# Performance work log

Hardware: AMD Instinct MI355X
Metric: run time of the kernel (lower is better)

Reference implementation:

```python
import jax, jax.numpy as jnp
import numpy as np

N_NODES = 50000
N_EDGES = 800000
FEAT = 128
HID = 128
NUM_GRAPHS = 64
ODE_STEPS = 8   # fixed-step RK4 stand-in for adaptive odeint over CFG.ode_time_points
DEPTH = 1.0
EPS = 1e-5


def layer_norm(x, g, b):
    m = jnp.mean(x, axis=-1, keepdims=True)
    v = jnp.var(x, axis=-1, keepdims=True)
    return (x - m) * jax.lax.rsqrt(v + EPS) * g + b


def setup_inputs() -> dict:
    key = jax.random.key(0)
    ks = jax.random.split(key, 16)
    s = 1.0 / np.sqrt(FEAT)
    sh = 1.0 / np.sqrt(HID)
    inp = {
        "x": jax.random.normal(ks[0], (N_NODES, FEAT), jnp.float32),
        "edge_index": jax.random.randint(ks[1], (2, N_EDGES), 0, N_NODES, jnp.int64),
        "batch": jnp.sort(jax.random.randint(ks[2], (N_NODES,), 0, NUM_GRAPHS, jnp.int64)),
        "alpha": jnp.float32(0.8),
        "beta": jnp.float32(0.6),
        "phase": jnp.float32(0.7),
        "W_in": jax.random.normal(ks[3], (FEAT, HID), jnp.float32) * s,
        "b_in": jnp.zeros((HID,), jnp.float32),
        "g_in": jnp.ones((HID,), jnp.float32),
        "be_in": jnp.zeros((HID,), jnp.float32),
        "W_alt": jax.random.normal(ks[4], (FEAT, HID), jnp.float32) * s,
        "b_alt": jnp.zeros((HID,), jnp.float32),
        "g_alt": jnp.ones((HID,), jnp.float32),
        "be_alt": jnp.zeros((HID,), jnp.float32),
        "W_self": jax.random.normal(ks[5], (HID, HID), jnp.float32) * sh,
        "W_msg": jax.random.normal(ks[6], (HID, HID), jnp.float32) * sh,
        "b_ode": jnp.zeros((HID,), jnp.float32),
        "W_int": jax.random.normal(ks[7], (2 * HID, HID), jnp.float32) * sh / np.sqrt(2.0),
        "b_int": jnp.zeros((HID,), jnp.float32),
        "g_int": jnp.ones((HID,), jnp.float32),
        "be_int": jnp.zeros((HID,), jnp.float32),
        "W_out": jax.random.normal(ks[8], (HID, HID), jnp.float32) * sh,
        "b_out": jnp.zeros((HID,), jnp.float32),
    }
    return inp


def _forward(x, alpha, beta, phase,
             W_in, b_in, g_in, be_in,
             W_alt, b_alt, g_alt, be_alt,
             W_self, W_msg, b_ode,
             W_int, b_int, g_int, be_int,
             W_out, b_out,
             edge_index, batch):
    src, dst = edge_index[0], edge_index[1]
    # in-degree for mean aggregation (clamped to 1)
    deg = jax.ops.segment_sum(jnp.ones((src.shape[0],), jnp.float32), dst,
                              num_segments=N_NODES)
    deg = jnp.maximum(deg, 1.0)[:, None]

    # quantum amplitudes -> measurement probabilities (normalized)
    norm = jnp.sqrt(alpha ** 2 + beta ** 2)
    a, b = alpha / norm, beta / norm
    p0, p1 = a ** 2, b ** 2

    # two projection pathways in superposition
    h0 = jax.nn.gelu(layer_norm(x @ W_in + b_in, g_in, be_in))
    h1 = jax.nn.gelu(layer_norm(x @ W_alt + b_alt, g_alt, be_alt))
    h = jnp.sqrt(p0) * h0 + jnp.sqrt(p1) * h1  # [N, H]

    # Neural ODE: dh/dt = tanh(h W_self + mean_{j->i}(h_j W_msg) + b)
    def ode_f(h):
        msg = h[src] @ W_msg                       # [E, H] gather + GEMM
        agg = jax.ops.segment_sum(msg, dst, num_segments=N_NODES) / deg
        return jnp.tanh(h @ W_self + agg + b_ode)

    dt = jnp.float32(DEPTH / ODE_STEPS)

    def rk4_step(h, _):
        k1 = ode_f(h)
        k2 = ode_f(h + 0.5 * dt * k1)
        k3 = ode_f(h + 0.5 * dt * k2)
        k4 = ode_f(h + dt * k3)
        return h + (dt / 6.0) * (k1 + 2.0 * k2 + 2.0 * k3 + k4), None

    h, _ = jax.lax.scan(rk4_step, h, None, length=ODE_STEPS)

    # quantum interference mixing (conditional branch -> masked add)
    interf = 2.0 * jnp.sqrt(p0 * p1) * jnp.cos(phase)
    h_int = jnp.tanh(layer_norm(jnp.concatenate([h, h], axis=-1) @ W_int + b_int,
                                g_int, be_int))
    gate = jnp.where(jnp.abs(interf) > 0.01, interf, 0.0)
    h = h + gate * h_int

    # eval-mode collapse: if p1 >= p0, scale by Re(e^{i*phase}) = cos(phase)
    h = jnp.where(p0 > p1, h, h * jnp.cos(phase))

    h_out = h @ W_out + b_out

    # global mean pool over graphs
    cnt = jax.ops.segment_sum(jnp.ones((N_NODES,), jnp.float32), batch,
                              num_segments=NUM_GRAPHS)
    pooled = jax.ops.segment_sum(h_out, batch, num_segments=NUM_GRAPHS)
    return pooled / jnp.maximum(cnt, 1.0)[:, None]  # [NUM_GRAPHS, H]


def reference(x, edge_index, batch, alpha, beta, phase,
              W_in, b_in, g_in, be_in,
              W_alt, b_alt, g_alt, be_alt,
              W_self, W_msg, b_ode,
              W_int, b_int, g_int, be_int,
              W_out, b_out):
    return _forward(x, alpha, beta, phase,
                    W_in, b_in, g_in, be_in,
                    W_alt, b_alt, g_alt, be_alt,
                    W_self, W_msg, b_ode,
                    W_int, b_int, g_int, be_int,
                    W_out, b_out, edge_index, batch)
```

## Files before the change

### kernel.cpp

```cpp
#include <hip/hip_runtime.h>
#include <math.h>

#define NND 50000
#define NED 800000
#define HD  128
#define NG  64
#define MT  32

typedef __attribute__((ext_vector_type(8))) short short8v;
typedef __attribute__((ext_vector_type(4))) float float4v;
typedef __attribute__((ext_vector_type(2))) float float2v;

__device__ __forceinline__ float gelu_t(float x) {
  const float c = 0.7978845608028654f;
  float t = tanhf(c * (x + 0.044715f * x * x * x));
  return 0.5f * x * (1.0f + t);
}

__device__ __forceinline__ unsigned short f2bf(float f) {
  unsigned int u = __float_as_uint(f);
  u += 0x7FFFu + ((u >> 16) & 1u);
  return (unsigned short)(u >> 16);
}
__device__ __forceinline__ float bf2f(unsigned short s) {
  return __uint_as_float(((unsigned int)s) << 16);
}
__device__ __forceinline__ float bflo(unsigned int u) { return __uint_as_float(u << 16); }
__device__ __forceinline__ float bfhi(unsigned int u) { return __uint_as_float(u & 0xFFFF0000u); }

__global__ void k_hist(const int* __restrict__ dst, int* __restrict__ degi) {
  int e = blockIdx.x * 256 + threadIdx.x;
  if (e < NED) atomicAdd(&degi[dst[e]], 1);
}

__global__ __launch_bounds__(1024) void k_scan(
    const int* __restrict__ degi, int* __restrict__ rowptr,
    int* __restrict__ cursor, float* __restrict__ deginv) {
  __shared__ int wsum[16];
  int tid = threadIdx.x;
  int lane = tid & 63;
  int wid = tid >> 6;
  int running = 0;
  for (int base = 0; base < NND; base += 1024) {
    int idx = base + tid;
    int v = (idx < NND) ? degi[idx] : 0;
    int s = v;
#pragma unroll
    for (int o = 1; o < 64; o <<= 1) {
      int t = __shfl_up(s, o, 64);
      if (lane >= o) s += t;
    }
    if (lane == 63) wsum[wid] = s;
    __syncthreads();
    if (wid == 0) {
      int ws = (lane < 16) ? wsum[lane] : 0;
#pragma unroll
      for (int o = 1; o < 16; o <<= 1) {
        int t = __shfl_up(ws, o, 64);
        if (lane >= o) ws += t;
      }
      if (lane < 16) wsum[lane] = ws;
    }
    __syncthreads();
    int woff = wid ? wsum[wid - 1] : 0;
    int excl = running + woff + s - v;
    if (idx < NND) {
      rowptr[idx] = excl;
      cursor[idx] = excl;
      deginv[idx] = 1.0f / (float)max(v, 1);
    }
    int tot = wsum[15];
    __syncthreads();
    running += tot;
  }
  if (tid == 0) rowptr[NND] = running;
}

__global__ void k_scatter(const int* __restrict__ src, const int* __restrict__ dst,
                          int* __restrict__ cursor, unsigned short* __restrict__ cs16) {
  int e = blockIdx.x * 256 + threadIdx.x;
  if (e < NED) {
    int d = dst[e];
    int pos = atomicAdd(&cursor[d], 1);
    cs16[pos] = (unsigned short)src[e];
  }
}

__global__ void k_cnt(const int* __restrict__ batch, float* __restrict__ cnt) {
  int g = threadIdx.x;
  if (g >= NG) return;
  int lo, hi, ub_g, ub_gm1;
  lo = 0; hi = NND;
  while (lo < hi) { int mid = (lo + hi) >> 1; if (batch[mid] <= g) lo = mid + 1; else hi = mid; }
  ub_g = lo;
  if (g == 0) ub_gm1 = 0;
  else {
    lo = 0; hi = NND;
    int v = g - 1;
    while (lo < hi) { int mid = (lo + hi) >> 1; if (batch[mid] <= v) lo = mid + 1; else hi = mid; }
    ub_gm1 = lo;
  }
  cnt[g] = (float)(ub_g - ub_gm1);
}

__global__ void k_weffT(const float* __restrict__ Wint, unsigned short* __restrict__ weffT) {
  int i = blockIdx.x * 256 + threadIdx.x;
  if (i < 128 * 128) {
    int n = i >> 7, k = i & 127;
    weffT[i] = f2bf(Wint[k * 128 + n] + Wint[(k + 128) * 128 + n]);
  }
}

__global__ void k_prepOut(const float* __restrict__ Wout, unsigned short* __restrict__ WoutT) {
  int i = blockIdx.x * 256 + threadIdx.x;
  if (i < 128 * 128) {
    int n = i >> 7, k = i & 127;
    WoutT[i] = f2bf(Wout[k * 128 + n]);
  }
}

__global__ void k_prepB(const float* __restrict__ Wself, const float* __restrict__ Wmsg,
                        unsigned short* __restrict__ Bt) {
  int i = blockIdx.x * 256 + threadIdx.x;
  if (i < 128 * 256) {
    int n = i >> 8, k = i & 255;
    float w = (k < HD) ? Wself[k * HD + n] : Wmsg[(k - HD) * HD + n];
    Bt[i] = f2bf(w);
  }
}

__global__ void k_prepIn(const float* __restrict__ Win, const float* __restrict__ Walt,
                         unsigned short* __restrict__ BtIn) {
  int i = blockIdx.x * 256 + threadIdx.x;
  if (i < 2 * 128 * 128) {
    int p = i >> 14; int rem = i & 16383; int n = rem >> 7; int k = rem & 127;
    const float* W = p ? Walt : Win;
    BtIn[i] = f2bf(W[k * 128 + n]);
  }
}

__global__ __launch_bounds__(256) void k_init2(
    const float* __restrict__ x, const unsigned short* __restrict__ BtIn,
    const float* __restrict__ bin, const float* __restrict__ gin, const float* __restrict__ bein,
    const float* __restrict__ balt, const float* __restrict__ galt, const float* __restrict__ bealt,
    const float* __restrict__ alphap, const float* __restrict__ betap,
    unsigned short* __restrict__ hbf)
{
  __shared__ float red[4][16][2];
  __shared__ unsigned short gtile[2][16][64];
  int tid = threadIdx.x;
  int wave = tid >> 6;
  int lane = tid & 63;
  int l15 = lane & 15;
  int lhi = lane >> 4;
  int path = wave >> 1;
  int colBase = (wave & 1) * 64;
  int rowBase = blockIdx.x * 64;

  const unsigned short* Bp = BtIn + path * 128 * 128;
  short8v bfr[4][4];
#pragma unroll
  for (int t = 0; t < 4; ++t) {
    int n = colBase + t * 16 + l15;
#pragma unroll
    for (int s = 0; s < 4; ++s)
      bfr[t][s] = *(const short8v*)&Bp[n * 128 + s * 32 + lhi * 8];
  }

  const float* bvp = path ? balt : bin;
  const float* gp  = path ? galt : gin;
  const float* bep = path ? bealt : bein;
  float bv[4], gw[4], bew[4];
#pragma unroll
  for (int t = 0; t < 4; ++t) {
    int col = colBase + t * 16 + l15;
    bv[t] = bvp[col]; gw[t] = gp[col]; bew[t] = bep[col];
  }

  float al = alphap[0], btv = betap[0];
  float nrm = sqrtf(al * al + btv * btv);
  float w0 = fabsf(al) / nrm, w1 = fabsf(btv) / nrm;

  for (int rt = 0; rt < 4; ++rt) {
    int arow = rowBase + rt * 16 + l15; if (arow >= NND) arow = NND - 1;
    short8v afr[4];
#pragma unroll
    for (int s = 0; s < 4; ++s) {
      float4 xa = *(const float4*)&x[(size_t)arow * HD + s * 32 + lhi * 8];
      float4 xb = *(const float4*)&x[(size_t)arow * HD + s * 32 + lhi * 8 + 4];
      short8v f;
      f[0] = (short)f2bf(xa.x); f[1] = (short)f2bf(xa.y);
      f[2] = (short)f2bf(xa.z); f[3] = (short)f2bf(xa.w);
      f[4] = (short)f2bf(xb.x); f[5] = (short)f2bf(xb.y);
      f[6] = (short)f2bf(xb.z); f[7] = (short)f2bf(xb.w);
      afr[s] = f;
    }

    float4v acc[4];
#pragma unroll
    for (int t = 0; t < 4; ++t) acc[t] = (float4v){0.f, 0.f, 0.f, 0.f};
#pragma unroll
    for (int s = 0; s < 4; ++s) {
#pragma unroll
      for (int t = 0; t < 4; ++t)
        acc[t] = __builtin_amdgcn_mfma_f32_16x16x32_bf16(afr[s], bfr[t][s], acc[t], 0, 0, 0);
    }

    float z[4][4];
    float psum[4], psq[4];
#pragma unroll
    for (int r = 0; r < 4; ++r) {
      float s1 = 0.f, s2 = 0.f;
#pragma unroll
      for (int t = 0; t < 4; ++t) {
        float zz = acc[t][r] + bv[t];
        z[r][t] = zz;
        s1 += zz; s2 += zz * zz;
      }
#pragma unroll
      for (int m = 1; m < 16; m <<= 1) {
        s1 += __shfl_xor(s1, m, 16);
        s2 += __shfl_xor(s2, m, 16);
      }
      psum[r] = s1; psq[r] = s2;
    }
    if (l15 == 0) {
#pragma unroll
      for (int r = 0; r < 4; ++r) {
        red[wave][lhi * 4 + r][0] = psum[r];
        red[wave][lhi * 4 + r][1] = psq[r];
      }
    }
    __syncthreads();

    int pw = wave ^ 1;
    float gval[4][4];
#pragma unroll
    for (int r = 0; r < 4; ++r) {
      int rowl = lhi * 4 + r;
      float S = psum[r] + red[pw][rowl][0];
      float Q = psq[r]  + red[pw][rowl][1];
      float mean = S * (1.0f / 128.0f);
      float var  = Q * (1.0f / 128.0f) - mean * mean;
      float rs = rsqrtf(var + 1e-5f);
#pragma unroll
      for (int t = 0; t < 4; ++t)
        gval[r][t] = gelu_t((z[r][t] - mean) * rs * gw[t] + bew[t]);
    }

    if (path == 1) {
#pragma unroll
      for (int r = 0; r < 4; ++r)
#pragma unroll
        for (int t = 0; t < 4; ++t)
          gtile[wave & 1][lhi * 4 + r][t * 16 + l15] = f2bf(gval[r][t]);
    }
    __syncthreads();

    if (path == 0) {
#pragma unroll
      for (int r = 0; r < 4; ++r) {
        int m = rowBase + rt * 16 + lhi * 4 + r;
        if (m < NND) {
#pragma unroll
          for (int t = 0; t < 4; ++t) {
            float g1 = bf2f(gtile[wave & 1][lhi * 4 + r][t * 16 + l15]);
            float hv = w0 * gval[r][t] + w1 * g1;
            hbf[(size_t)m * HD + colBase + t * 16 + l15] = f2bf(hv);
          }
        }
      }
    }
    __syncthreads();
  }
}

__global__ __launch_bounds__(256) void k_gath2(
    const unsigned short* __restrict__ hbf,
    const unsigned char*  __restrict__ t8,
    unsigned short* __restrict__ usav,
    unsigned short* __restrict__ uT,
    const int* __restrict__ rowptr,
    const unsigned short* __restrict__ cs16,
    const float* __restrict__ deginv,
    int mode, float cu)
{
  int tid = threadIdx.x;
  int l16 = tid & 15;
  int grp = tid >> 4;
  int node = blockIdx.x * 16 + grp;
  if (node >= NND) return;
  int e0 = rowptr[node], e1 = rowptr[node + 1];
  float a0=0,a1=0,a2=0,a3=0,a4=0,a5=0,a6=0,a7=0;

  if (mode == 0) {
    for (int eb = e0; eb < e1; eb += 16) {
      int rem = e1 - eb;
      int ia = eb + l16; if (ia > e1 - 1) ia = e1 - 1;
      int my = cs16[ia];
      int n16 = (rem < 16) ? rem : 16;
#pragma unroll
      for (int j = 0; j < 16; ++j) {
        if (j < n16) {
          int s = __shfl(my, j, 16);
          uint4 v = *(const uint4*)&hbf[(size_t)s * HD + l16 * 8];
          a0 += bflo(v.x); a1 += bfhi(v.x); a2 += bflo(v.y); a3 += bfhi(v.y);
          a4 += bflo(v.z); a5 += bfhi(v.z); a6 += bflo(v.w); a7 += bfhi(v.w);
        }
      }
    }
  } else {
    for (int eb = e0; eb < e1; eb += 16) {
      int rem = e1 - eb;
      int ia = eb + l16; if (ia > e1 - 1) ia = e1 - 1;
      int my = cs16[ia];
      int n16 = (rem < 16) ? rem : 16;
      uint2 v[16];
#pragma unroll
      for (int j = 0; j < 16; ++j) {
        if (j < n16) {
          int s = __shfl(my, j, 16);
          v[j] = *(const uint2*)&t8[(size_t)s * HD + l16 * 8];
        }
      }
#pragma unroll
      for (int j = 0; j < 16; ++j) {
        if (j < n16) {
          float2v f0 = __builtin_amdgcn_cvt_pk_f32_fp8(v[j].x, false);
          float2v f1 = __builtin_amdgcn_cvt_pk_f32_fp8(v[j].x, true);
          float2v f2 = __builtin_amdgcn_cvt_pk_f32_fp8(v[j].y, false);
          float2v f3 = __builtin_amdgcn_cvt_pk_f32_fp8(v[j].y, true);
          a0 += f0[0]; a1 += f0[1]; a2 += f1[0]; a3 += f1[1];
          a4 += f2[0]; a5 += f2[1]; a6 += f3[0]; a7 += f3[1];
        }
      }
    }
  }

  float sc = deginv[node] * ((mode == 0) ? 1.0f : ((mode == 1) ? 0.125f : cu));
  size_t base = (size_t)node * HD + l16 * 8;
  float u0,u1,u2,u3,u4,u5,u6,u7;
  if (mode == 0) {
    u0=a0*sc; u1=a1*sc; u2=a2*sc; u3=a3*sc; u4=a4*sc; u5=a5*sc; u6=a6*sc; u7=a7*sc;
  } else {
    uint4 us = *(const uint4*)&usav[base];
    u0 = bflo(us.x) + a0*sc; u1 = bfhi(us.x) + a1*sc;
    u2 = bflo(us.y) + a2*sc; u3 = bfhi(us.y) + a3*sc;
    u4 = bflo(us.z) + a4*sc; u5 = bfhi(us.z) + a5*sc;
    u6 = bflo(us.w) + a6*sc; u7 = bfhi(us.w) + a7*sc;
  }
  uint4 o;
  o.x = (unsigned int)f2bf(u0) | ((unsigned int)f2bf(u1) << 16);
  o.y = (unsigned int)f2bf(u2) | ((unsigned int)f2bf(u3) << 16);
  o.z = (unsigned int)f2bf(u4) | ((unsigned int)f2bf(u5) << 16);
  o.w = (unsigned int)f2bf(u6) | ((unsigned int)f2bf(u7) << 16);
  if (mode <= 1) *(uint4*)&usav[base] = o;
  *(uint4*)&uT[base] = o;
}

__global__ __launch_bounds__(256) void k_ode2(
    const unsigned short* __restrict__ ain,
    unsigned short* __restrict__ hbf,
    const unsigned short* __restrict__ uT,
    unsigned char* __restrict__ k8w,
    const unsigned char* __restrict__ k8r0,
    const unsigned char* __restrict__ k8r1,
    const unsigned char* __restrict__ k8r2,
    unsigned char* __restrict__ dh8,
    const unsigned short* __restrict__ Bt, const float* __restrict__ bode,
    unsigned short* __restrict__ ybf, int stage)
{
  int tid = threadIdx.x;
  int wave = tid >> 6;
  int lane = tid & 63;
  int l15 = lane & 15;
  int lhi = lane >> 4;
  int rowBase = blockIdx.x * MT;
  int ncol0 = wave * 32;

  const float DT = 0.125f;
  const float cy = (stage <= 1) ? 0.5f * DT : DT;
  const float w6 = DT / 6.0f;

  short8v bfr[2][8];
#pragma unroll
  for (int t = 0; t < 2; ++t) {
    int n = ncol0 + t * 16 + l15;
#pragma unroll
    for (int s = 0; s < 8; ++s) {
      bfr[t][s] = *(const short8v*)&Bt[n * 256 + s * 32 + lhi * 8];
    }
  }
  float4 bo4[2];
  bo4[0] = *(const float4*)&bode[ncol0 + lhi * 4];
  bo4[1] = *(const float4*)&bode[ncol0 + 16 + lhi * 4];

#pragma unroll
  for (int rt = 0; rt < MT / 16; ++rt) {
    int mload = rowBase + rt * 16 + l15;
    if (mload >= NND) mload = NND - 1;
    short8v afr[8];
#pragma unroll
    for (int s = 0; s < 4; ++s)
      afr[s] = *(const short8v*)&ain[(size_t)mload * HD + s * 32 + lhi * 8];
#pragma unroll
    for (int s = 0; s < 4; ++s)
      afr[4 + s] = *(const short8v*)&uT[(size_t)mload * HD + s * 32 + lhi * 8];

    float4v acc0 = {0.f, 0.f, 0.f, 0.f};
    float4v acc1 = {0.f, 0.f, 0.f, 0.f};
#pragma unroll
    for (int s = 0; s < 8; ++s) {
      acc0 = __builtin_amdgcn_mfma_f32_16x16x32_bf16(bfr[0][s], afr[s], acc0, 0, 0, 0);
      acc1 = __builtin_amdgcn_mfma_f32_16x16x32_bf16(bfr[1][s], afr[s], acc1, 0, 0, 0);
    }

    int m = rowBase + rt * 16 + l15;
    if (m < NND) {
#pragma unroll
      for (int t = 0; t < 2; ++t) {
        int n0 = ncol0 + t * 16 + lhi * 4;
        size_t off = (size_t)m * HD + n0;
        float4v acc = t ? acc1 : acc0;
        float4 bo = bo4[t];
        float kv0 = tanhf(acc[0] + bo.x);
        float kv1 = tanhf(acc[1] + bo.y);
        float kv2 = tanhf(acc[2] + bo.z);
        float kv3 = tanhf(acc[3] + bo.w);
        if (stage < 3) {
          uint2 hv = *(const uint2*)&hbf[off];
          float y0 = bflo(hv.x) + cy * kv0;
          float y1 = bfhi(hv.x) + cy * kv1;
          float y2 = bflo(hv.y) + cy * kv2;
          float y3 = bfhi(hv.y) + cy * kv3;
          uint2 yo;
          yo.x = (unsigned int)f2bf(y0) | ((unsigned int)f2bf(y1) << 16);
          yo.y = (unsigned int)f2bf(y2) | ((unsigned int)f2bf(y3) << 16);
          *(uint2*)&ybf[off] = yo;
          unsigned int p8 = __builtin_amdgcn_cvt_pk_fp8_f32(kv0, kv1, 0u, false);
          p8 = __builtin_amdgcn_cvt_pk_fp8_f32(kv2, kv3, p8, true);
          *(unsigned int*)&k8w[off] = p8;
        } else {
          unsigned int q0 = *(const unsigned int*)&k8r0[off];
          unsigned int q1 = *(const unsigned int*)&k8r1[off];
          unsigned int q2 = *(const unsigned int*)&k8r2[off];
          float2v a0 = __builtin_amdgcn_cvt_pk_f32_fp8(q0, false);
          float2v a1 = __builtin_amdgcn_cvt_pk_f32_fp8(q0, true);
          float2v b0 = __builtin_amdgcn_cvt_pk_f32_fp8(q1, false);
          float2v b1 = __builtin_amdgcn_cvt_pk_f32_fp8(q1, true);
          float2v c0 = __builtin_amdgcn_cvt_pk_f32_fp8(q2, false);
          float2v c1 = __builtin_amdgcn_cvt_pk_f32_fp8(q2, true);
          float dh0 = w6 * (a0[0] + 2.f * b0[0] + 2.f * c0[0] + kv0);
          float dh1 = w6 * (a0[1] + 2.f * b0[1] + 2.f * c0[1] + kv1);
          float dh2 = w6 * (a1[0] + 2.f * b1[0] + 2.f * c1[0] + kv2);
          float dh3 = w6 * (a1[1] + 2.f * b1[1] + 2.f * c1[1] + kv3);
          uint2 hv = *(const uint2*)&hbf[off];
          float h0 = bflo(hv.x) + dh0;
          float h1 = bfhi(hv.x) + dh1;
          float h2 = bflo(hv.y) + dh2;
          float h3 = bfhi(hv.y) + dh3;
          uint2 ho;
          ho.x = (unsigned int)f2bf(h0) | ((unsigned int)f2bf(h1) << 16);
          ho.y = (unsigned int)f2bf(h2) | ((unsigned int)f2bf(h3) << 16);
          *(uint2*)&hbf[off] = ho;
          unsigned int p8 = __builtin_amdgcn_cvt_pk_fp8_f32(8.0f * dh0, 8.0f * dh1, 0u, false);
          p8 = __builtin_amdgcn_cvt_pk_fp8_f32(8.0f * dh2, 8.0f * dh3, p8, true);
          *(unsigned int*)&dh8[off] = p8;
        }
      }
    }
  }
}

__global__ __launch_bounds__(256) void k_interf2(
    const unsigned short* __restrict__ hbf, const unsigned short* __restrict__ weffT,
    const float* __restrict__ bint, const float* __restrict__ gint,
    const float* __restrict__ beint,
    const float* __restrict__ alphap, const float* __restrict__ betap,
    const float* __restrict__ phasep,
    unsigned short* __restrict__ h2bf)
{
  __shared__ float red[4][16][2];
  int tid = threadIdx.x;
  int wave = tid >> 6;
  int lane = tid & 63;
  int l15 = lane & 15;
  int lhi = lane >> 4;
  int rowBase = blockIdx.x * 32;
  int ncol0 = wave * 32;

  short8v bfr[2][4];
#pragma unroll
  for (int t = 0; t < 2; ++t) {
    int n = ncol0 + t * 16 + l15;
#pragma unroll
    for (int s = 0; s < 4; ++s)
      bfr[t][s] = *(const short8v*)&weffT[n * 128 + s * 32 + lhi * 8];
  }
  float4 bi4[2], gv4[2], bev4[2];
#pragma unroll
  for (int t = 0; t < 2; ++t) {
    int n0 = ncol0 + t * 16 + lhi * 4;
    bi4[t]  = *(const float4*)&bint[n0];
    gv4[t]  = *(const float4*)&gint[n0];
    bev4[t] = *(const float4*)&beint[n0];
  }

  float al = alphap[0], bt = betap[0], ph = phasep[0];
  float n2 = al*al + bt*bt;
  float p0 = (al*al) / n2, p1 = (bt*bt) / n2;
  float interf = 2.0f * sqrtf(p0 * p1) * cosf(ph);
  float gate = (fabsf(interf) > 0.01f) ? interf : 0.0f;
  float cscale = (p0 > p1) ? 1.0f : cosf(ph);

  for (int rt = 0; rt < 2; ++rt) {
    int mload = rowBase + rt * 16 + l15;
    if (mload >= NND) mload = NND - 1;
    short8v afr[4];
#pragma unroll
    for (int s = 0; s < 4; ++s)
      afr[s] = *(const short8v*)&hbf[(size_t)mload * HD + s * 32 + lhi * 8];

    float4v acc0 = {0.f, 0.f, 0.f, 0.f};
    float4v acc1 = {0.f, 0.f, 0.f, 0.f};
#pragma unroll
    for (int s = 0; s < 4; ++s) {
      acc0 = __builtin_amdgcn_mfma_f32_16x16x32_bf16(bfr[0][s], afr[s], acc0, 0, 0, 0);
      acc1 = __builtin_amdgcn_mfma_f32_16x16x32_bf16(bfr[1][s], afr[s], acc1, 0, 0, 0);
    }

    float z[2][4];
    float s1 = 0.f, s2 = 0.f;
#pragma unroll
    for (int t = 0; t < 2; ++t) {
      float4v acc = t ? acc1 : acc0;
#pragma unroll
      for (int i = 0; i < 4; ++i) {
        float zz = acc[i] + ((const float*)&bi4[t])[i];
        z[t][i] = zz;
        s1 += zz; s2 += zz * zz;
      }
    }
    s1 += __shfl_xor(s1, 16, 64); s2 += __shfl_xor(s2, 16, 64);
    s1 += __shfl_xor(s1, 32, 64); s2 += __shfl_xor(s2, 32, 64);
    if (lhi == 0) { red[wave][l15][0] = s1; red[wave][l15][1] = s2; }
    __syncthreads();
    float S = red[0][l15][0] + red[1][l15][0] + red[2][l15][0] + red[3][l15][0];
    float Q = red[0][l15][1] + red[1][l15][1] + red[2][l15][1] + red[3][l15][1];
    float mean = S * (1.0f / 128.0f);
    float var  = Q * (1.0f / 128.0f) - mean * mean;
    float rs = rsqrtf(var + 1e-5f);

    int m = rowBase + rt * 16 + l15;
    if (m < NND) {
#pragma unroll
      for (int t = 0; t < 2; ++t) {
        size_t off = (size_t)m * HD + ncol0 + t * 16 + lhi * 4;
        uint2 hv = *(const uint2*)&hbf[off];
        float h0 = bflo(hv.x), h1 = bfhi(hv.x), h2 = bflo(hv.y), h3 = bfhi(hv.y);
        float t0 = tanhf((z[t][0]-mean)*rs*((const float*)&gv4[t])[0] + ((const float*)&bev4[t])[0]);
        float t1 = tanhf((z[t][1]-mean)*rs*((const float*)&gv4[t])[1] + ((const float*)&bev4[t])[1]);
        float t2 = tanhf((z[t][2]-mean)*rs*((const float*)&gv4[t])[2] + ((const float*)&bev4[t])[2]);
        float t3 = tanhf((z[t][3]-mean)*rs*((const float*)&gv4[t])[3] + ((const float*)&bev4[t])[3]);
        float o0 = (h0 + gate*t0) * cscale;
        float o1 = (h1 + gate*t1) * cscale;
        float o2 = (h2 + gate*t2) * cscale;
        float o3 = (h3 + gate*t3) * cscale;
        uint2 oo;
        oo.x = (unsigned int)f2bf(o0) | ((unsigned int)f2bf(o1) << 16);
        oo.y = (unsigned int)f2bf(o2) | ((unsigned int)f2bf(o3) << 16);
        *(uint2*)&h2bf[off] = oo;
      }
    }
    __syncthreads();
  }
}

__global__ __launch_bounds__(256) void k_out2(
    const unsigned short* __restrict__ h2bf, const unsigned short* __restrict__ WoutT,
    const float* __restrict__ bout, const int* __restrict__ batch,
    float* __restrict__ pooled)
{
  __shared__ float lpool[2][128];
  __shared__ int lgid[2];
  int tid = threadIdx.x;
  int wave = tid >> 6;
  int lane = tid & 63;
  int l15 = lane & 15;
  int lhi = lane >> 4;
  int rowBase = blockIdx.x * 32;
  int ncol0 = wave * 32;

  lpool[tid >> 7][tid & 127] = 0.f;
  if (tid == 0) {
    lgid[0] = batch[rowBase < NND ? rowBase : NND - 1];
    int last = rowBase + 31; if (last >= NND) last = NND - 1;
    lgid[1] = batch[last];
  }
  __syncthreads();

  short8v bfr[2][4];
#pragma unroll
  for (int t = 0; t < 2; ++t) {
    int n = ncol0 + t * 16 + l15;
#pragma unroll
    for (int s = 0; s < 4; ++s)
      bfr[t][s] = *(const short8v*)&WoutT[n * 128 + s * 32 + lhi * 8];
  }
  float4 bo4[2];
  bo4[0] = *(const float4*)&bout[ncol0 + lhi * 4];
  bo4[1] = *(const float4*)&bout[ncol0 + 16 + lhi * 4];

#pragma unroll
  for (int rt = 0; rt < 2; ++rt) {
    int mload = rowBase + rt * 16 + l15;
    if (mload >= NND) mload = NND - 1;
    short8v afr[4];
#pragma unroll
    for (int s = 0; s < 4; ++s)
      afr[s] = *(const short8v*)&h2bf[(size_t)mload * HD + s * 32 + lhi * 8];

    float4v acc0 = {0.f, 0.f, 0.f, 0.f};
    float4v acc1 = {0.f, 0.f, 0.f, 0.f};
#pragma unroll
    for (int s = 0; s < 4; ++s) {
      acc0 = __builtin_amdgcn_mfma_f32_16x16x32_bf16(bfr[0][s], afr[s], acc0, 0, 0, 0);
      acc1 = __builtin_amdgcn_mfma_f32_16x16x32_bf16(bfr[1][s], afr[s], acc1, 0, 0, 0);
    }

    int m = rowBase + rt * 16 + l15;
    if (m < NND) {
      int g = batch[m];
      int slot = (g == lgid[0]) ? 0 : 1;
#pragma unroll
      for (int t = 0; t < 2; ++t) {
        int n0 = ncol0 + t * 16 + lhi * 4;
        float4v acc = t ? acc1 : acc0;
        float4 bo = bo4[t];
        atomicAdd(&lpool[slot][n0 + 0], acc[0] + bo.x);
        atomicAdd(&lpool[slot][n0 + 1], acc[1] + bo.y);
        atomicAdd(&lpool[slot][n0 + 2], acc[2] + bo.z);
        atomicAdd(&lpool[slot][n0 + 3], acc[3] + bo.w);
      }
    }
  }
  __syncthreads();
  int slot = tid >> 7, col = tid & 127;
  if (slot == 0 || lgid[1] != lgid[0])
    atomicAdd(&pooled[lgid[slot] * HD + col], lpool[slot][col]);
}

__global__ void k_final(const float* __restrict__ pooled, const float* __restrict__ cnt,
                        float* __restrict__ out) {
  int i = blockIdx.x * 256 + threadIdx.x;
  if (i < NG * HD) out[i] = pooled[i] / fmaxf(cnt[i >> 7], 1.0f);
}

extern "C" void kernel_launch(void* const* d_in, const int* in_sizes, int n_in,
                              void* d_out, int out_size, void* d_ws, size_t ws_size,
                              hipStream_t stream) {
  (void)in_sizes; (void)n_in; (void)out_size; (void)ws_size;
  const float* x     = (const float*)d_in[0];
  const int*   ei    = (const int*)d_in[1];
  const int*   batch = (const int*)d_in[2];
  const float* alpha = (const float*)d_in[3];
  const float* beta  = (const float*)d_in[4];
  const float* phase = (const float*)d_in[5];
  const float* Win   = (const float*)d_in[6];
  const float* bin   = (const float*)d_in[7];
  const float* gin   = (const float*)d_in[8];
  const float* bein  = (const float*)d_in[9];
  const float* Walt  = (const float*)d_in[10];
  const float* balt  = (const float*)d_in[11];
  const float* galt  = (const float*)d_in[12];
  const float* bealt = (const float*)d_in[13];
  const float* Wself = (const float*)d_in[14];
  const float* Wmsg  = (const float*)d_in[15];
  const float* bode  = (const float*)d_in[16];
  const float* Wint  = (const float*)d_in[17];
  const float* bint  = (const float*)d_in[18];
  const float* gint  = (const float*)d_in[19];
  const float* beint = (const float*)d_in[20];
  const float* Wout  = (const float*)d_in[21];
  const float* bout  = (const float*)d_in[22];
  float* out = (float*)d_out;

  const int* esrc = ei;
  const int* edst = ei + NED;

  size_t NH = (size_t)NND * HD;
  float* deginv = (float*)d_ws;
  float* pooled = deginv + NND;
  float* cnt    = pooled + NG * HD;
  unsigned short* hbf   = (unsigned short*)(cnt + NG);
  unsigned short* ybf   = hbf + NH;
  unsigned short* usav  = ybf + NH;
  unsigned short* uT    = usav + NH;
  unsigned short* h2bf  = uT + NH;
  unsigned short* Bt    = h2bf + NH;
  unsigned short* BtIn  = Bt + 128 * 256;
  unsigned short* weffT = BtIn + 2 * 128 * 128;
  unsigned short* WoutT = weffT + 128 * 128;
  unsigned short* cs16  = WoutT + 128 * 128;
  unsigned char* k80 = (unsigned char*)(cs16 + NED);
  unsigned char* k81 = k80 + NH;
  unsigned char* k82 = k81 + NH;
  unsigned char* dh8 = k82 + NH;
  int* degi   = (int*)(dh8 + NH);
  int* rowptr = degi + NND;
  int* cursor = rowptr + (NND + 4);

  hipMemsetAsync(degi, 0, NND * sizeof(int), stream);
  hipMemsetAsync(pooled, 0, NG * HD * sizeof(float), stream);

  k_hist   <<<(NED + 255) / 256, 256, 0, stream>>>(edst, degi);
  k_scan   <<<1, 1024, 0, stream>>>(degi, rowptr, cursor, deginv);
  k_scatter<<<(NED + 255) / 256, 256, 0, stream>>>(esrc, edst, cursor, cs16);
  k_cnt    <<<1, 64, 0, stream>>>(batch, cnt);
  k_weffT  <<<64, 256, 0, stream>>>(Wint, weffT);
  k_prepOut<<<64, 256, 0, stream>>>(Wout, WoutT);
  k_prepB  <<<128, 256, 0, stream>>>(Wself, Wmsg, Bt);
  k_prepIn <<<128, 256, 0, stream>>>(Win, Walt, BtIn);
  k_init2  <<<(NND + 63) / 64, 256, 0, stream>>>(x, BtIn, bin, gin, bein,
                                                 balt, galt, bealt,
                                                 alpha, beta, hbf);

  const float DT = 0.125f;
  int gg = (NND + 15) / 16;
  int ob = (NND + MT - 1) / MT;
  for (int step = 0; step < 8; ++step) {
    k_gath2<<<gg, 256, 0, stream>>>(hbf, dh8, usav, uT, rowptr, cs16, deginv,
                                    (step == 0) ? 0 : 1, 0.f);
    k_ode2 <<<ob, 256, 0, stream>>>(hbf, hbf, uT, k80, k80, k81, k82, dh8,
                                    Bt, bode, ybf, 0);
    k_gath2<<<gg, 256, 0, stream>>>(hbf, k80, usav, uT, rowptr, cs16, deginv, 2, 0.5f * DT);
    k_ode2 <<<ob, 256, 0, stream>>>(ybf, hbf, uT, k81, k80, k81, k82, dh8,
                                    Bt, bode, ybf, 1);
    k_gath2<<<gg, 256, 0, stream>>>(hbf, k81, usav, uT, rowptr, cs16, deginv, 2, 0.5f * DT);
    k_ode2 <<<ob, 256, 0, stream>>>(ybf, hbf, uT, k82, k80, k81, k82, dh8,
                                    Bt, bode, ybf, 2);
    k_gath2<<<gg, 256, 0, stream>>>(hbf, k82, usav, uT, rowptr, cs16, deginv, 2, DT);
    k_ode2 <<<ob, 256, 0, stream>>>(ybf, hbf, uT, k80, k80, k81, k82, dh8,
                                    Bt, bode, ybf, 3);
  }
  k_interf2<<<(NND + 31) / 32, 256, 0, stream>>>(hbf, weffT, bint, gint, beint,
                                                 alpha, beta, phase, h2bf);
  k_out2  <<<(NND + 31) / 32, 256, 0, stream>>>(h2bf, WoutT, bout, batch, pooled);
  k_final <<<(NG * HD + 255) / 256, 256, 0, stream>>>(pooled, cnt, out);
}
```

Baseline: 2.150 ms.

## Recompute RK4 stage input from fp8 k, and pool before the output projection

The ODE kernel no longer writes the intermediate y = h + c*k buffer in bf16. The next stage rebuilds it from h and the fp8 k tensor while loading its inputs, which cuts a bf16 write and read per stage. The h state is now ping-ponged between two buffers. The output projection is moved after mean pooling (linearity): per-graph row sums are reduced first, then a tiny 64x128x128 matmul with a bias scaled by count replaces the per-node MFMA and atomics. A risk is that k_rowsum runs only 64 blocks, so occupancy is low for a 12.8 MB read.

```diff
diff --git a/kernel.cpp b/kernel.cpp
--- a/kernel.cpp
+++ b/kernel.cpp
@@ -86,21 +86,23 @@
   }
 }
 
-__global__ void k_cnt(const int* __restrict__ batch, float* __restrict__ cnt) {
+__global__ void k_cnt(const int* __restrict__ batch, float* __restrict__ cnt,
+                      int* __restrict__ rowstart) {
   int g = threadIdx.x;
   if (g >= NG) return;
-  int lo, hi, ub_g, ub_gm1;
-  lo = 0; hi = NND;
+  int lo = 0, hi = NND;
   while (lo < hi) { int mid = (lo + hi) >> 1; if (batch[mid] <= g) lo = mid + 1; else hi = mid; }
-  ub_g = lo;
-  if (g == 0) ub_gm1 = 0;
-  else {
+  int ub_g = lo;
+  int ub_gm1 = 0;
+  if (g > 0) {
     lo = 0; hi = NND;
     int v = g - 1;
     while (lo < hi) { int mid = (lo + hi) >> 1; if (batch[mid] <= v) lo = mid + 1; else hi = mid; }
     ub_gm1 = lo;
   }
   cnt[g] = (float)(ub_g - ub_gm1);
+  rowstart[g + 1] = ub_g;
+  if (g == 0) rowstart[0] = 0;
 }
 
 __global__ void k_weffT(const float* __restrict__ Wint, unsigned short* __restrict__ weffT) {
@@ -108,14 +110,6 @@
   if (i < 128 * 128) {
     int n = i >> 7, k = i & 127;
     weffT[i] = f2bf(Wint[k * 128 + n] + Wint[(k + 128) * 128 + n]);
-  }
-}
-
-__global__ void k_prepOut(const float* __restrict__ Wout, unsigned short* __restrict__ WoutT) {
-  int i = blockIdx.x * 256 + threadIdx.x;
-  if (i < 128 * 128) {
-    int n = i >> 7, k = i & 127;
-    WoutT[i] = f2bf(Wout[k * 128 + n]);
   }
 }
 
@@ -358,17 +352,18 @@
   *(uint4*)&uT[base] = o;
 }
 
-__global__ __launch_bounds__(256) void k_ode2(
-    const unsigned short* __restrict__ ain,
-    unsigned short* __restrict__ hbf,
+__global__ __launch_bounds__(256) void k_ode3(
+    const unsigned short* __restrict__ hc,
+    unsigned short* __restrict__ hn,
     const unsigned short* __restrict__ uT,
+    const unsigned char* __restrict__ k8A,
     unsigned char* __restrict__ k8w,
     const unsigned char* __restrict__ k8r0,
     const unsigned char* __restrict__ k8r1,
     const unsigned char* __restrict__ k8r2,
     unsigned char* __restrict__ dh8,
     const unsigned short* __restrict__ Bt, const float* __restrict__ bode,
-    unsigned short* __restrict__ ybf, int stage)
+    int stage, float cyA)
 {
   int tid = threadIdx.x;
   int wave = tid >> 6;
@@ -379,7 +374,6 @@
   int ncol0 = wave * 32;
 
   const float DT = 0.125f;
-  const float cy = (stage <= 1) ? 0.5f * DT : DT;
   const float w6 = DT / 6.0f;
 
   short8v bfr[2][8];
@@ -401,8 +395,29 @@
     if (mload >= NND) mload = NND - 1;
     short8v afr[8];
 #pragma unroll
-    for (int s = 0; s < 4; ++s)
-      afr[s] = *(const short8v*)&ain[(size_t)mload * HD + s * 32 + lhi * 8];
+    for (int s = 0; s < 4; ++s) {
+      size_t base = (size_t)mload * HD + s * 32 + lhi * 8;
+      if (stage == 0) {
+        afr[s] = *(const short8v*)&hc[base];
+      } else {
+        uint4 hv = *(const uint4*)&hc[base];
+        uint2 kq = *(const uint2*)&k8A[base];
+        float2v f0 = __builtin_amdgcn_cvt_pk_f32_fp8(kq.x, false);
+        float2v f1 = __builtin_amdgcn_cvt_pk_f32_fp8(kq.x, true);
+        float2v f2 = __builtin_amdgcn_cvt_pk_f32_fp8(kq.y, false);
+        float2v f3 = __builtin_amdgcn_cvt_pk_f32_fp8(kq.y, true);
+        short8v f;
+        f[0] = (short)f2bf(bflo(hv.x) + cyA * f0[0]);
+        f[1] = (short)f2bf(bfhi(hv.x) + cyA * f0[1]);
+        f[2] = (short)f2bf(bflo(hv.y) + cyA * f1[0]);
+        f[3] = (short)f2bf(bfhi(hv.y) + cyA * f1[1]);
+        f[4] = (short)f2bf(bflo(hv.z) + cyA * f2[0]);
+        f[5] = (short)f2bf(bfhi(hv.z) + cyA * f2[1]);
+        f[6] = (short)f2bf(bflo(hv.w) + cyA * f3[0]);
+        f[7] = (short)f2bf(bfhi(hv.w) + cyA * f3[1]);
+        afr[s] = f;
+      }
+    }
 #pragma unroll
     for (int s = 0; s < 4; ++s)
       afr[4 + s] = *(const short8v*)&uT[(size_t)mload * HD + s * 32 + lhi * 8];
@@ -428,15 +443,6 @@
         float kv2 = tanhf(acc[2] + bo.z);
         float kv3 = tanhf(acc[3] + bo.w);
         if (stage < 3) {
-          uint2 hv = *(const uint2*)&hbf[off];
-          float y0 = bflo(hv.x) + cy * kv0;
-          float y1 = bfhi(hv.x) + cy * kv1;
-          float y2 = bflo(hv.y) + cy * kv2;
-          float y3 = bfhi(hv.y) + cy * kv3;
-          uint2 yo;
-          yo.x = (unsigned int)f2bf(y0) | ((unsigned int)f2bf(y1) << 16);
-          yo.y = (unsigned int)f2bf(y2) | ((unsigned int)f2bf(y3) << 16);
-          *(uint2*)&ybf[off] = yo;
           unsigned int p8 = __builtin_amdgcn_cvt_pk_fp8_f32(kv0, kv1, 0u, false);
           p8 = __builtin_amdgcn_cvt_pk_fp8_f32(kv2, kv3, p8, true);
           *(unsigned int*)&k8w[off] = p8;
@@ -454,7 +460,7 @@
           float dh1 = w6 * (a0[1] + 2.f * b0[1] + 2.f * c0[1] + kv1);
           float dh2 = w6 * (a1[0] + 2.f * b1[0] + 2.f * c1[0] + kv2);
           float dh3 = w6 * (a1[1] + 2.f * b1[1] + 2.f * c1[1] + kv3);
-          uint2 hv = *(const uint2*)&hbf[off];
+          uint2 hv = *(const uint2*)&hc[off];
           float h0 = bflo(hv.x) + dh0;
           float h1 = bfhi(hv.x) + dh1;
           float h2 = bflo(hv.y) + dh2;
@@ -462,7 +468,7 @@
           uint2 ho;
           ho.x = (unsigned int)f2bf(h0) | ((unsigned int)f2bf(h1) << 16);
           ho.y = (unsigned int)f2bf(h2) | ((unsigned int)f2bf(h3) << 16);
-          *(uint2*)&hbf[off] = ho;
+          *(uint2*)&hn[off] = ho;
           unsigned int p8 = __builtin_amdgcn_cvt_pk_fp8_f32(8.0f * dh0, 8.0f * dh1, 0u, false);
           p8 = __builtin_amdgcn_cvt_pk_fp8_f32(8.0f * dh2, 8.0f * dh3, p8, true);
           *(unsigned int*)&dh8[off] = p8;
@@ -576,84 +582,50 @@
   }
 }
 
-__global__ __launch_bounds__(256) void k_out2(
-    const unsigned short* __restrict__ h2bf, const unsigned short* __restrict__ WoutT,
-    const float* __restrict__ bout, const int* __restrict__ batch,
-    float* __restrict__ pooled)
+__global__ __launch_bounds__(256) void k_rowsum(
+    const unsigned short* __restrict__ h2bf, const int* __restrict__ rowstart,
+    float* __restrict__ sg)
 {
-  __shared__ float lpool[2][128];
-  __shared__ int lgid[2];
-  int tid = threadIdx.x;
-  int wave = tid >> 6;
-  int lane = tid & 63;
-  int l15 = lane & 15;
-  int lhi = lane >> 4;
-  int rowBase = blockIdx.x * 32;
-  int ncol0 = wave * 32;
-
-  lpool[tid >> 7][tid & 127] = 0.f;
-  if (tid == 0) {
-    lgid[0] = batch[rowBase < NND ? rowBase : NND - 1];
-    int last = rowBase + 31; if (last >= NND) last = NND - 1;
-    lgid[1] = batch[last];
-  }
+  __shared__ float red[8][128];
+  int g = blockIdx.x;
+  int r0 = rowstart[g], r1 = rowstart[g + 1];
+  int colq = threadIdx.x & 31;
+  int rowp = threadIdx.x >> 5;
+  float a0 = 0.f, a1 = 0.f, a2 = 0.f, a3 = 0.f;
+  for (int r = r0 + rowp; r < r1; r += 8) {
+    uint2 v = *(const uint2*)&h2bf[(size_t)r * HD + colq * 4];
+    a0 += bflo(v.x); a1 += bfhi(v.x); a2 += bflo(v.y); a3 += bfhi(v.y);
+  }
+  red[rowp][colq * 4 + 0] = a0;
+  red[rowp][colq * 4 + 1] = a1;
+  red[rowp][colq * 4 + 2] = a2;
+  red[rowp][colq * 4 + 3] = a3;
   __syncthreads();
-
-  short8v bfr[2][4];
-#pragma unroll
-  for (int t = 0; t < 2; ++t) {
-    int n = ncol0 + t * 16 + l15;
-#pragma unroll
-    for (int s = 0; s < 4; ++s)
-      bfr[t][s] = *(const short8v*)&WoutT[n * 128 + s * 32 + lhi * 8];
-  }
-  float4 bo4[2];
-  bo4[0] = *(const float4*)&bout[ncol0 + lhi * 4];
-  bo4[1] = *(const float4*)&bout[ncol0 + 16 + lhi * 4];
-
-#pragma unroll
-  for (int rt = 0; rt < 2; ++rt) {
-    int mload = rowBase + rt * 16 + l15;
-    if (mload >= NND) mload = NND - 1;
-    short8v afr[4];
-#pragma unroll
-    for (int s = 0; s < 4; ++s)
-      afr[s] = *(const short8v*)&h2bf[(size_t)mload * HD + s * 32 + lhi * 8];
-
-    float4v acc0 = {0.f, 0.f, 0.f, 0.f};
-    float4v acc1 = {0.f, 0.f, 0.f, 0.f};
-#pragma unroll
-    for (int s = 0; s < 4; ++s) {
-      acc0 = __builtin_amdgcn_mfma_f32_16x16x32_bf16(bfr[0][s], afr[s], acc0, 0, 0, 0);
-      acc1 = __builtin_amdgcn_mfma_f32_16x16x32_bf16(bfr[1][s], afr[s], acc1, 0, 0, 0);
-    }
-
-    int m = rowBase + rt * 16 + l15;
-    if (m < NND) {
-      int g = batch[m];
-      int slot = (g == lgid[0]) ? 0 : 1;
-#pragma unroll
-      for (int t = 0; t < 2; ++t) {
-        int n0 = ncol0 + t * 16 + lhi * 4;
-        float4v acc = t ? acc1 : acc0;
-        float4 bo = bo4[t];
-        atomicAdd(&lpool[slot][n0 + 0], acc[0] + bo.x);
-        atomicAdd(&lpool[slot][n0 + 1], acc[1] + bo.y);
-        atomicAdd(&lpool[slot][n0 + 2], acc[2] + bo.z);
-        atomicAdd(&lpool[slot][n0 + 3], acc[3] + bo.w);
-      }
-    }
-  }
+  if (rowp == 0) {
+#pragma unroll
+    for (int i = 0; i < 4; ++i) {
+      int c = colq * 4 + i;
+      float s = red[0][c] + red[1][c] + red[2][c] + red[3][c]
+              + red[4][c] + red[5][c] + red[6][c] + red[7][c];
+      sg[g * HD + c] = s;
+    }
+  }
+}
+
+__global__ __launch_bounds__(128) void k_pool(
+    const float* __restrict__ sg, const float* __restrict__ Wout,
+    const float* __restrict__ bout, const float* __restrict__ cnt,
+    float* __restrict__ out)
+{
+  __shared__ float srow[128];
+  int g = blockIdx.x;
+  int c = threadIdx.x;
+  srow[c] = sg[g * HD + c];
   __syncthreads();
-  int slot = tid >> 7, col = tid & 127;
-  if (slot == 0 || lgid[1] != lgid[0])
-    atomicAdd(&pooled[lgid[slot] * HD + col], lpool[slot][col]);
-}
-
-__global__ void k_final(const float* __restrict__ pooled, const float* __restrict__ cnt,
-                        float* __restrict__ out) {
-  int i = blockIdx.x * 256 + threadIdx.x;
-  if (i < NG * HD) out[i] = pooled[i] / fmaxf(cnt[i >> 7], 1.0f);
+  float s = 0.f;
+  for (int k = 0; k < 128; ++k) s += srow[k] * Wout[k * HD + c];
+  float cg = cnt[g];
+  out[g * HD + c] = (s + cg * bout[c]) / fmaxf(cg, 1.0f);
 }
 
 extern "C" void kernel_launch(void* const* d_in, const int* in_sizes, int n_in,
@@ -690,61 +662,62 @@
 
   size_t NH = (size_t)NND * HD;
   float* deginv = (float*)d_ws;
-  float* pooled = deginv + NND;
-  float* cnt    = pooled + NG * HD;
-  unsigned short* hbf   = (unsigned short*)(cnt + NG);
-  unsigned short* ybf   = hbf + NH;
-  unsigned short* usav  = ybf + NH;
+  float* cnt    = deginv + NND;
+  float* sg     = cnt + NG;
+  unsigned short* hA    = (unsigned short*)(sg + NG * HD);
+  unsigned short* hB    = hA + NH;
+  unsigned short* usav  = hB + NH;
   unsigned short* uT    = usav + NH;
   unsigned short* h2bf  = uT + NH;
   unsigned short* Bt    = h2bf + NH;
   unsigned short* BtIn  = Bt + 128 * 256;
   unsigned short* weffT = BtIn + 2 * 128 * 128;
-  unsigned short* WoutT = weffT + 128 * 128;
-  unsigned short* cs16  = WoutT + 128 * 128;
+  unsigned short* cs16  = weffT + 128 * 128;
   unsigned char* k80 = (unsigned char*)(cs16 + NED);
   unsigned char* k81 = k80 + NH;
   unsigned char* k82 = k81 + NH;
   unsigned char* dh8 = k82 + NH;
-  int* degi   = (int*)(dh8 + NH);
-  int* rowptr = degi + NND;
-  int* cursor = rowptr + (NND + 4);
+  int* degi     = (int*)(dh8 + NH);
+  int* rowptr   = degi + NND;
+  int* cursor   = rowptr + (NND + 4);
+  int* rowstart = cursor + NND;
 
   hipMemsetAsync(degi, 0, NND * sizeof(int), stream);
-  hipMemsetAsync(pooled, 0, NG * HD * sizeof(float), stream);
 
   k_hist   <<<(NED + 255) / 256, 256, 0, stream>>>(edst, degi);
   k_scan   <<<1, 1024, 0, stream>>>(degi, rowptr, cursor, deginv);
   k_scatter<<<(NED + 255) / 256, 256, 0, stream>>>(esrc, edst, cursor, cs16);
-  k_cnt    <<<1, 64, 0, stream>>>(batch, cnt);
+  k_cnt    <<<1, 64, 0, stream>>>(batch, cnt, rowstart);
   k_weffT  <<<64, 256, 0, stream>>>(Wint, weffT);
-  k_prepOut<<<64, 256, 0, stream>>>(Wout, WoutT);
   k_prepB  <<<128, 256, 0, stream>>>(Wself, Wmsg, Bt);
   k_prepIn <<<128, 256, 0, stream>>>(Win, Walt, BtIn);
   k_init2  <<<(NND + 63) / 64, 256, 0, stream>>>(x, BtIn, bin, gin, bein,
                                                  balt, galt, bealt,
-                                                 alpha, beta, hbf);
+                                                 alpha, beta, hA);
 
   const float DT = 0.125f;
   int gg = (NND + 15) / 16;
   int ob = (NND + MT - 1) / MT;
+  unsigned short* hcur = hA;
+  unsigned short* hnext = hB;
   for (int step = 0; step < 8; ++step) {
-    k_gath2<<<gg, 256, 0, stream>>>(hbf, dh8, usav, uT, rowptr, cs16, deginv,
+    k_gath2<<<gg, 256, 0, stream>>>(hcur, dh8, usav, uT, rowptr, cs16, deginv,
                                     (step == 0) ? 0 : 1, 0.f);
-    k_ode2 <<<ob, 256, 0, stream>>>(hbf, hbf, uT, k80, k80, k81, k82, dh8,
-                                    Bt, bode, ybf, 0);
-    k_gath2<<<gg, 256, 0, stream>>>(hbf, k80, usav, uT, rowptr, cs16, deginv, 2, 0.5f * DT);
-    k_ode2 <<<ob, 256, 0, stream>>>(ybf, hbf, uT, k81, k80, k81, k82, dh8,
-                                    Bt, bode, ybf, 1);
-    k_gath2<<<gg, 256, 0, stream>>>(hbf, k81, usav, uT, rowptr, cs16, deginv, 2, 0.5f * DT);
-    k_ode2 <<<ob, 256, 0, stream>>>(ybf, hbf, uT, k82, k80, k81, k82, dh8,
-                                    Bt, bode, ybf, 2);
-    k_gath2<<<gg, 256, 0, stream>>>(hbf, k82, usav, uT, rowptr, cs16, deginv, 2, DT);
-    k_ode2 <<<ob, 256, 0, stream>>>(ybf, hbf, uT, k80, k80, k81, k82, dh8,
-                                    Bt, bode, ybf, 3);
-  }
-  k_interf2<<<(NND + 31) / 32, 256, 0, stream>>>(hbf, weffT, bint, gint, beint,
+    k_ode3 <<<ob, 256, 0, stream>>>(hcur, hnext, uT, k80, k80, k80, k81, k82, dh8,
+                                    Bt, bode, 0, 0.f);
+    k_gath2<<<gg, 256, 0, stream>>>(hcur, k80, usav, uT, rowptr, cs16, deginv, 2, 0.5f * DT);
+    k_ode3 <<<ob, 256, 0, stream>>>(hcur, hnext, uT, k80, k81, k80, k81, k82, dh8,
+                                    Bt, bode, 1, 0.5f * DT);
+    k_gath2<<<gg, 256, 0, stream>>>(hcur, k81, usav, uT, rowptr, cs16, deginv, 2, 0.5f * DT);
+    k_ode3 <<<ob, 256, 0, stream>>>(hcur, hnext, uT, k81, k82, k80, k81, k82, dh8,
+                                    Bt, bode, 2, 0.5f * DT);
+    k_gath2<<<gg, 256, 0, stream>>>(hcur, k82, usav, uT, rowptr, cs16, deginv, 2, DT);
+    k_ode3 <<<ob, 256, 0, stream>>>(hcur, hnext, uT, k82, k80, k80, k81, k82, dh8,
+                                    Bt, bode, 3, DT);
+    unsigned short* tmp = hcur; hcur = hnext; hnext = tmp;
+  }
+  k_interf2<<<(NND + 31) / 32, 256, 0, stream>>>(hcur, weffT, bint, gint, beint,
                                                  alpha, beta, phase, h2bf);
-  k_out2  <<<(NND + 31) / 32, 256, 0, stream>>>(h2bf, WoutT, bout, batch, pooled);
-  k_final <<<(NG * HD + 255) / 256, 256, 0, stream>>>(pooled, cnt, out);
-}
+  k_rowsum<<<NG, 256, 0, stream>>>(h2bf, rowstart, sg);
+  k_pool  <<<NG, 128, 0, stream>>>(sg, Wout, bout, cnt, out);
+}
```

Result: no change. 2.127 ms (-1.0%).
